# Optimization experiments

Measured on AMD Instinct MI355X. Metric: run time of the kernel, lower is better.

The kernel has to match this reference:

```python
import jax, jax.numpy as jnp
import numpy as np

N_HEADS = 12
N_GROUPS = 32
EPS = 1e-5


def setup_inputs() -> dict:
    key = jax.random.key(0)
    ks = jax.random.split(key, 6)
    B, C, H, W = 8, 768, 32, 32
    EC, S = 768, 256
    x = jax.random.normal(ks[0], (B, C, H, W), dtype=jnp.float32)
    encoder_out = jax.random.normal(ks[1], (B, EC, S), dtype=jnp.float32)
    gn_w = jnp.ones((C,), jnp.float32)
    gn_b = jnp.zeros((C,), jnp.float32)
    qkv_w = jax.random.normal(ks[2], (3 * C, C), dtype=jnp.float32) * 0.02
    qkv_b = jnp.zeros((3 * C,), jnp.float32)
    enc_w = jax.random.normal(ks[3], (2 * C, EC), dtype=jnp.float32) * 0.02
    enc_b = jnp.zeros((2 * C,), jnp.float32)
    proj_w = jax.random.normal(ks[4], (C, C), dtype=jnp.float32) * 0.02
    proj_b = jnp.zeros((C,), jnp.float32)
    return {"x": x, "encoder_out": encoder_out, "gn_w": gn_w, "gn_b": gn_b,
            "qkv_w": qkv_w, "qkv_b": qkv_b, "enc_w": enc_w, "enc_b": enc_b,
            "proj_w": proj_w, "proj_b": proj_b}


def _group_norm(x, w, b):
    # x: [B, C, T]
    B, C, T = x.shape
    xg = x.reshape(B, N_GROUPS, C // N_GROUPS, T)
    mean = jnp.mean(xg, axis=(2, 3), keepdims=True)
    var = jnp.var(xg, axis=(2, 3), keepdims=True)
    xn = ((xg - mean) * jax.lax.rsqrt(var + EPS)).reshape(B, C, T)
    return xn * w[None, :, None] + b[None, :, None]


def reference(x, encoder_out, gn_w, gn_b, qkv_w, qkv_b, enc_w, enc_b, proj_w, proj_b):
    B, C, Hs, Ws = x.shape
    T = Hs * Ws
    ch = C // N_HEADS
    xf = x.reshape(B, C, T)
    xn = _group_norm(xf, gn_w, gn_b)
    # 1x1 conv == channel matmul
    qkv = jnp.einsum('oc,bct->bot', qkv_w, xn) + qkv_b[None, :, None]  # [B, 3C, T]
    # torch layout: per-head contiguous blocks of [q, k, v]
    qkv = qkv.reshape(B * N_HEADS, 3 * ch, T)
    q, k, v = qkv[:, :ch], qkv[:, ch:2 * ch], qkv[:, 2 * ch:]
    ekv = jnp.einsum('oc,bcs->bos', enc_w, encoder_out) + enc_b[None, :, None]  # [B, 2C, S]
    ekv = ekv.reshape(B * N_HEADS, 2 * ch, -1)
    ek, ev = ekv[:, :ch], ekv[:, ch:]
    k = jnp.concatenate([ek, k], axis=-1)  # [BH, ch, S+T]
    v = jnp.concatenate([ev, v], axis=-1)
    scale = 1.0 / np.sqrt(np.sqrt(ch))
    w = jnp.einsum('bct,bcs->bts', q * scale, k * scale)  # [BH, T, S+T]
    w = jax.nn.softmax(w.astype(jnp.float32), axis=-1).astype(q.dtype)
    a = jnp.einsum('bts,bcs->bct', w, v).reshape(B, C, T)
    h = jnp.einsum('oc,bct->bot', proj_w, a) + proj_b[None, :, None]
    return (xf + h).reshape(B, C, Hs, Ws)
```

## Files before the change

kernel.cpp:

```cpp
#include <hip/hip_runtime.h>

typedef __attribute__((ext_vector_type(8))) short bf16x8;
typedef __attribute__((ext_vector_type(4))) float f32x4;
typedef __attribute__((ext_vector_type(16))) float f32x16;
typedef __attribute__((ext_vector_type(4))) float float4v;
typedef __attribute__((ext_vector_type(4))) unsigned short ushort4v;
typedef __attribute__((ext_vector_type(8))) unsigned short ushort8v;

#define DEVINL __device__ __forceinline__


DEVINL unsigned short f2bf(float f) {
  union { float f; unsigned u; } v; v.f = f;
  unsigned r = (v.u + 0x7fffu + ((v.u >> 16) & 1u)) >> 16;
  return (unsigned short)r;
}
DEVINL float bf2f(unsigned short h) {
  union { unsigned u; float f; } v; v.u = ((unsigned)h) << 16;
  return v.f;
}
DEVINL float exp2a(float x) {
  float r; asm("v_exp_f32 %0, %1" : "=v"(r) : "v"(x)); return r;
}
DEVINL unsigned cvtpk(float lo, float hi) {
  unsigned r;
  asm("v_cvt_pk_bf16_f32 %0, %1, %2" : "=v"(r) : "v"(lo), "v"(hi));
  return r;
}
DEVINL void gload16(const void* g, void* l) {
  __builtin_amdgcn_global_load_lds(
      (const __attribute__((address_space(1))) unsigned*)g,
      (__attribute__((address_space(3))) unsigned*)l, 16, 0, 0);
}
DEVINL void plswap(unsigned& a, unsigned& b) {
  asm("v_permlane32_swap_b32 %0, %1" : "+v"(a), "+v"(b));
}
DEVINL bf16x8 mkfrag(unsigned a, unsigned b, unsigned c, unsigned d) {
  union { unsigned u[4]; bf16x8 v; } x;
  x.u[0] = a; x.u[1] = b; x.u[2] = c; x.u[3] = d;
  return x.v;
}
#define WAITV0 asm volatile("s_waitcnt vmcnt(0)" ::: "memory")
#define RBAR  __builtin_amdgcn_s_barrier()

__global__ __launch_bounds__(256) void k_cvt3(const float* __restrict__ s0,
                                              const float* __restrict__ s1,
                                              const float* __restrict__ s2,
                                              unsigned short* __restrict__ d) {
  int i = blockIdx.x * 256 + threadIdx.x;
  const float* s; int off;
  if (i < 442368)      { s = s0; off = i; }
  else if (i < 737280) { s = s1; off = i - 442368; }
  else                 { s = s2; off = i - 737280; }
  float4v v = *(const float4v*)(s + (size_t)off * 4);
  ushort4v o;
  o[0] = f2bf(v[0]); o[1] = f2bf(v[1]); o[2] = f2bf(v[2]); o[3] = f2bf(v[3]);
  *(ushort4v*)(d + (size_t)i * 4) = o;
}

__global__ __launch_bounds__(256) void k_gn(const float* __restrict__ x,
                                            const float* __restrict__ gw,
                                            const float* __restrict__ gb,
                                            unsigned short* __restrict__ xnt) {
  int g = blockIdx.x, b = blockIdx.y, tid = threadIdx.x;
  const float* xb = x + ((size_t)b * 768 + g * 24) * 1024;
  float s = 0.f, ss = 0.f;
  for (int i = tid; i < 6144; i += 256) {
    float4v v = *(const float4v*)(xb + (size_t)i * 4);
    s += v[0] + v[1] + v[2] + v[3];
    ss += v[0] * v[0] + v[1] * v[1] + v[2] * v[2] + v[3] * v[3];
  }
  #pragma unroll
  for (int o = 32; o > 0; o >>= 1) { s += __shfl_down(s, o); ss += __shfl_down(ss, o); }
  __shared__ float rs[4], rss[4], stat[2];
  int w = tid >> 6;
  if ((tid & 63) == 0) { rs[w] = s; rss[w] = ss; }
  __syncthreads();
  if (tid == 0) {
    float S = rs[0] + rs[1] + rs[2] + rs[3], SS = rss[0] + rss[1] + rss[2] + rss[3];
    float mean = S / 24576.f;
    float var = SS / 24576.f - mean * mean;
    stat[0] = mean; stat[1] = rsqrtf(fmaxf(var, 0.f) + 1e-5f);
  }
  __syncthreads();
  float mean = stat[0], rstd = stat[1];
  float wv[24], bv[24];
  #pragma unroll
  for (int c = 0; c < 24; ++c) { wv[c] = gw[g * 24 + c]; bv[c] = gb[g * 24 + c]; }
  for (int it = 0; it < 4; ++it) {
    int t = it * 256 + tid;
    ushort8v ov[3];
    #pragma unroll
    for (int c = 0; c < 24; ++c) {
      float v = xb[(size_t)c * 1024 + t];
      ov[c >> 3][c & 7] = f2bf((v - mean) * rstd * wv[c] + bv[c]);
    }
    ushort8v* dst = (ushort8v*)(xnt + ((size_t)(b * 1024 + t)) * 768 + g * 24);
    dst[0] = ov[0]; dst[1] = ov[1]; dst[2] = ov[2];
  }
}

__global__ __launch_bounds__(256) void k_enc_tr(const float* __restrict__ enc,
                                                unsigned short* __restrict__ et) {
  int ct = blockIdx.x * 64, st = blockIdx.y * 64, b = blockIdx.z, tid = threadIdx.x;
  __shared__ unsigned short L[64 * 72];
  #pragma unroll
  for (int it = 0; it < 4; ++it) {
    int idx = it * 256 + tid; int r = idx >> 4, ch = idx & 15;
    float4v v = *(const float4v*)(enc + ((size_t)(b * 768 + ct + r)) * 256 + st + ch * 4);
    ushort4v o;
    o[0] = f2bf(v[0]); o[1] = f2bf(v[1]); o[2] = f2bf(v[2]); o[3] = f2bf(v[3]);
    *(ushort4v*)&L[r * 72 + ch * 4] = o;
  }
  __syncthreads();
  #pragma unroll
  for (int it = 0; it < 2; ++it) {
    int idx = it * 256 + tid; int s = idx >> 3, ch = idx & 7;
    ushort8v o;
    #pragma unroll
    for (int j = 0; j < 8; ++j) o[j] = L[(ch * 8 + j) * 72 + s];
    *(ushort8v*)(et + ((size_t)(b * 256 + st + s)) * 768 + ct + ch * 8) = o;
  }
}

__global__ __launch_bounds__(256) void k_vcat(const unsigned short* __restrict__ qkvt,
                                              const unsigned short* __restrict__ ekvt,
                                              unsigned short* __restrict__ vcat) {
  int s0 = blockIdx.x * 64, bh = blockIdx.y, b = bh / 12, h = bh % 12, tid = threadIdx.x;
  __shared__ unsigned short L[64 * 72];
  #pragma unroll
  for (int it = 0; it < 2; ++it) {
    int idx = it * 256 + tid; int s = idx >> 3, ch = idx & 7;
    int sg = s0 + s;
    const unsigned short* src = (sg < 256)
        ? ekvt + ((size_t)(b * 256 + sg)) * 1536 + h * 128 + 64 + ch * 8
        : qkvt + ((size_t)(b * 1024 + sg - 256)) * 2304 + h * 192 + 128 + ch * 8;
    *(ushort8v*)&L[s * 72 + ch * 8] = *(const ushort8v*)src;
  }
  __syncthreads();
  #pragma unroll
  for (int it = 0; it < 2; ++it) {
    int idx = it * 256 + tid; int c = idx >> 3, ch = idx & 7;
    ushort8v o;
    #pragma unroll
    for (int j = 0; j < 8; ++j) o[j] = L[(ch * 8 + j) * 72 + c];
    *(ushort8v*)(vcat + ((size_t)bh * 64 + c) * 1280 + s0 + ch * 8) = o;
  }
}

template <int EPI, int BM>
__global__ __launch_bounds__(256, 3) void k_gemm(const unsigned short* __restrict__ A,
                                                 const unsigned short* __restrict__ B,
                                                 const float* __restrict__ bias,
                                                 const float* __restrict__ resid,
                                                 void* __restrict__ outp,
                                                 int N, int K,
                                                 long sA, long sB, long sO, long sR) {
  constexpr int R32 = BM / 64;
  int bz = blockIdx.z;
  int m0 = blockIdx.x * BM, n0 = blockIdx.y * 128;
  const unsigned short* Ab = A + (size_t)bz * sA + (size_t)m0 * K;
  const unsigned short* Bb = B + (size_t)bz * sB + (size_t)n0 * K;
  __shared__ unsigned short As[3][BM * 32], Bs[3][128 * 32];
  int tid = threadIdx.x, lane = tid & 63, w = tid >> 6;
  int l31 = lane & 31, hi2 = lane >> 5;
  int wm = (w >> 1) * (BM / 2), wn = (w & 1) * 64;
  int sr = tid >> 2, sc = tid & 3;
  int schunk = (sc ^ ((sr >> 1) & 3)) * 8;
  const unsigned short* gA = Ab + (size_t)sr * K + schunk;
  const unsigned short* gB = Bb + (size_t)sr * K + schunk;

  f32x16 acc[R32][2];
  #pragma unroll
  for (int i = 0; i < R32; ++i)
    #pragma unroll
    for (int j = 0; j < 2; ++j)
      #pragma unroll
      for (int r = 0; r < 16; ++r) acc[i][j][r] = 0.f;

  auto stageAB = [&](int buf, int k0) {
    unsigned short* ad = &As[buf][0] + w * 512;
    unsigned short* bd = &Bs[buf][0] + w * 512;
    gload16(gA + k0, ad);
    if constexpr (BM == 128) gload16(gA + (size_t)64 * K + k0, ad + 2048);
    gload16(gB + k0, bd);
    gload16(gB + (size_t)64 * K + k0, bd + 2048);
  };
  auto WAITP = [&] {
    if constexpr (BM == 128) asm volatile("s_waitcnt vmcnt(4)" ::: "memory");
    else                     asm volatile("s_waitcnt vmcnt(3)" ::: "memory");
  };
  auto comp = [&](int buf) {
    const char* abase = (const char*)&As[buf][0];
    const char* bbase = (const char*)&Bs[buf][0];
    #pragma unroll
    for (int kk = 0; kk < 2; ++kk) {
      bf16x8 afr[R32], bfr[2];
      #pragma unroll
      for (int ri = 0; ri < R32; ++ri) {
        int row = wm + ri * 32 + l31;
        int sl = (kk * 2 + hi2) ^ ((row >> 1) & 3);
        afr[ri] = *(const bf16x8*)(abase + row * 64 + sl * 16);
      }
      #pragma unroll
      for (int ci = 0; ci < 2; ++ci) {
        int row = wn + ci * 32 + l31;
        int sl = (kk * 2 + hi2) ^ ((row >> 1) & 3);
        bfr[ci] = *(const bf16x8*)(bbase + row * 64 + sl * 16);
      }
      #pragma unroll
      for (int ri = 0; ri < R32; ++ri)
        #pragma unroll
        for (int ci = 0; ci < 2; ++ci)
          acc[ri][ci] = __builtin_amdgcn_mfma_f32_32x32x16_bf16(afr[ri], bfr[ci],
                                                                acc[ri][ci], 0, 0, 0);
    }
  };

  int nk = K >> 5;
  stageAB(0, 0);
  stageAB(1, 32);
  WAITP();
  RBAR;
  int cur = 0;
  for (int kt = 0; kt < nk - 2; ++kt) {
    int pre = cur - 1; if (pre < 0) pre += 3;
    stageAB(pre, (kt + 2) * 32);
    comp(cur);
    WAITP();
    RBAR;
    ++cur; if (cur == 3) cur = 0;
  }
  comp(cur);
  WAITV0;
  RBAR;
  ++cur; if (cur == 3) cur = 0;
  comp(cur);

  #pragma unroll
  for (int ri = 0; ri < R32; ++ri) {
    #pragma unroll
    for (int ci = 0; ci < 2; ++ci) {
      #pragma unroll
      for (int rg = 0; rg < 16; ++rg) {
        int row = m0 + wm + ri * 32 + (rg & 3) + 8 * (rg >> 2) + 4 * hi2;
        int col = n0 + wn + ci * 32 + l31;
        float v = acc[ri][ci][rg];
        if (EPI == 0) {
          v += bias[col];
          ((unsigned short*)outp)[(size_t)bz * sO + (size_t)row * N + col] = f2bf(v);
        } else {
          v += bias[row] + resid[(size_t)bz * sR + (size_t)row * N + col];
          ((float*)outp)[(size_t)bz * sO + (size_t)row * N + col] = v;
        }
      }
    }
  }
}

__global__ __launch_bounds__(256, 3) void k_attn(const unsigned short* __restrict__ qkvt,
                                                 const unsigned short* __restrict__ ekvt,
                                                 const unsigned short* __restrict__ vcat,
                                                 unsigned short* __restrict__ at) {
  int bid = blockIdx.x;
  int swb = (bid & 7) * 96 + (bid >> 3);
  int t0 = (swb & 7) * 128, bh = swb >> 3, b = bh / 12, h = bh % 12;
  int tid = threadIdx.x, w = tid >> 6, lane = tid & 63;
  int ql = lane & 31, hi = lane >> 5;
  __shared__ unsigned short Ks[2][4096], Vs[2][4096];

  const float QSC = 0.125f * 1.44269504089f;
  bf16x8 aq[4];
  const unsigned short* qrow = qkvt + ((size_t)(b * 1024 + t0 + w * 32 + ql)) * 2304 + h * 192;
  #pragma unroll
  for (int jc = 0; jc < 4; ++jc) {
    ushort8v qv = *(const ushort8v*)(qrow + jc * 16 + hi * 8);
    bf16x8 o;
    #pragma unroll
    for (int e = 0; e < 8; ++e) o[e] = (short)f2bf(bf2f(qv[e]) * QSC);
    aq[jc] = o;
  }

  int rloc = w * 16 + (lane >> 3);
  int chunk = (lane & 7) ^ (lane >> 3);
  const unsigned short* ke_st = ekvt + ((size_t)(b * 256 + rloc)) * 1536 + h * 128 + chunk * 8;
  const unsigned short* kq_st = qkvt + ((long)b * 1024 - 256 + rloc) * 2304 + h * 192 + 64 + chunk * 8;
  const unsigned short* v_st  = vcat + ((size_t)(bh * 64 + rloc)) * 1280 + chunk * 8;
  unsigned short* kd = &Ks[0][0] + w * 1024;
  unsigned short* vd = &Vs[0][0] + w * 1024;

  auto stage = [&](int nb, int tn) {
    const unsigned short* ks;
    size_t rstep;
    if (tn < 4) { ks = ke_st + (size_t)tn * 64 * 1536; rstep = 8 * 1536; }
    else        { ks = kq_st + (size_t)tn * 64 * 2304; rstep = 8 * 2304; }
    unsigned short* kdd = kd + nb * 4096;
    unsigned short* vdd = vd + nb * 4096;
    const unsigned short* vs = v_st + tn * 64;
    gload16(ks, kdd);
    gload16(ks + rstep, kdd + 512);
    gload16(vs, vdd);
    gload16(vs + 8 * 1280, vdd + 512);
  };

  stage(0, 0);
  WAITV0;
  __syncthreads();

  f32x16 acc0, acc1;
  #pragma unroll
  for (int r = 0; r < 16; ++r) { acc0[r] = 0.f; acc1[r] = 0.f; }
  float l = 0.f;
  int xp = (ql & 7) << 4;

  for (int t = 0; t < 20; ++t) {
    int cur = t & 1;
    if (t < 19) stage(cur ^ 1, t + 1);

    f32x16 sf0, sf1;
    #pragma unroll
    for (int r = 0; r < 16; ++r) { sf0[r] = 0.f; sf1[r] = 0.f; }
    const char* kbase = (const char*)&Ks[cur][0] + ql * 128;
    __builtin_amdgcn_s_setprio(1);
    #pragma unroll
    for (int jc = 0; jc < 4; ++jc) {
      int off = (jc * 32 + hi * 16) ^ xp;
      bf16x8 k0f = *(const bf16x8*)(kbase + off);
      bf16x8 k1f = *(const bf16x8*)(kbase + 4096 + off);
      sf0 = __builtin_amdgcn_mfma_f32_32x32x16_bf16(k0f, aq[jc], sf0, 0, 0, 0);
      sf1 = __builtin_amdgcn_mfma_f32_32x32x16_bf16(k1f, aq[jc], sf1, 0, 0, 0);
    }
    __builtin_amdgcn_s_setprio(0);

    float pe[32];
    #pragma unroll
    for (int i = 0; i < 16; ++i) pe[i] = exp2a(sf0[i]);
    #pragma unroll
    for (int i = 0; i < 16; ++i) pe[16 + i] = exp2a(sf1[i]);

    const char* vbase = (const char*)&Vs[cur][0] + ql * 128;
    #pragma unroll
    for (int sb = 0; sb < 2; ++sb) {
      unsigned pk[8];
      #pragma unroll
      for (int i = 0; i < 8; ++i)
        pk[i] = cvtpk(pe[sb * 16 + 2 * i], pe[sb * 16 + 2 * i + 1]);
      plswap(pk[0], pk[2]);
      plswap(pk[1], pk[3]);
      plswap(pk[4], pk[6]);
      plswap(pk[5], pk[7]);
      bf16x8 fj0 = mkfrag(pk[0], pk[1], pk[2], pk[3]);
      bf16x8 fj1 = mkfrag(pk[4], pk[5], pk[6], pk[7]);
      __builtin_amdgcn_s_setprio(1);
      #pragma unroll
      for (int jj = 0; jj < 2; ++jj) {
        int off = (sb * 64 + jj * 32 + hi * 16) ^ xp;
        bf16x8 v0f = *(const bf16x8*)(vbase + off);
        bf16x8 v1f = *(const bf16x8*)(vbase + 4096 + off);
        bf16x8 pf = jj ? fj1 : fj0;
        acc0 = __builtin_amdgcn_mfma_f32_32x32x16_bf16(v0f, pf, acc0, 0, 0, 0);
        acc1 = __builtin_amdgcn_mfma_f32_32x32x16_bf16(v1f, pf, acc1, 0, 0, 0);
      }
      __builtin_amdgcn_s_setprio(0);
    }

    float s0 = 0.f, s1 = 0.f, s2 = 0.f, s3 = 0.f;
    #pragma unroll
    for (int i = 0; i < 8; ++i) {
      s0 += pe[i]; s1 += pe[8 + i]; s2 += pe[16 + i]; s3 += pe[24 + i];
    }
    l += (s0 + s1) + (s2 + s3);

    if (t < 19) WAITV0;
    __syncthreads();
  }

  l += __shfl_xor(l, 32);
  float rl = 1.f / l;
  unsigned short* orow = at + ((size_t)(b * 1024 + t0 + w * 32 + ql)) * 768 + h * 64;
  #pragma unroll
  for (int cb = 0; cb < 2; ++cb) {
    #pragma unroll
    for (int g = 0; g < 4; ++g) {
      int c = cb * 32 + g * 8 + hi * 4;
      ushort4v o;
      #pragma unroll
      for (int i = 0; i < 4; ++i) {
        float v = (cb ? acc1[g * 4 + i] : acc0[g * 4 + i]) * rl;
        o[i] = f2bf(v);
      }
      *(ushort4v*)(orow + c) = o;
    }
  }
}

extern "C" void kernel_launch(void* const* d_in, const int* in_sizes, int n_in,
                              void* d_out, int out_size, void* d_ws, size_t ws_size,
                              hipStream_t stream) {
  const float* x      = (const float*)d_in[0];
  const float* enc    = (const float*)d_in[1];
  const float* gn_w   = (const float*)d_in[2];
  const float* gn_b   = (const float*)d_in[3];
  const float* qkv_w  = (const float*)d_in[4];
  const float* qkv_b  = (const float*)d_in[5];
  const float* enc_w  = (const float*)d_in[6];
  const float* enc_b  = (const float*)d_in[7];
  const float* proj_w = (const float*)d_in[8];
  const float* proj_b = (const float*)d_in[9];
  float* out = (float*)d_out;

  char* ws = (char*)d_ws;
  unsigned short* w_qkv = (unsigned short*)(ws + 0);
  unsigned short* w_enc = (unsigned short*)(ws + 3538944);
  unsigned short* w_prj = (unsigned short*)(ws + 5898240);
  unsigned short* xn_t  = (unsigned short*)(ws + 7077888);
  unsigned short* enc_t = (unsigned short*)(ws + 19660800);
  unsigned short* qkv_t = (unsigned short*)(ws + 22806528);
  unsigned short* ekv_t = (unsigned short*)(ws + 60555264);
  unsigned short* vcat  = (unsigned short*)(ws + 66846720);
  unsigned short* a_t   = xn_t;

  k_cvt3<<<3456, 256, 0, stream>>>(qkv_w, enc_w, proj_w, w_qkv);
  k_gn<<<dim3(32, 8), 256, 0, stream>>>(x, gn_w, gn_b, xn_t);
  k_enc_tr<<<dim3(12, 4, 8), 256, 0, stream>>>(enc, enc_t);
  k_gemm<0, 128><<<dim3(64, 18, 1), 256, 0, stream>>>(xn_t, w_qkv, qkv_b, nullptr, qkv_t,
                                                      2304, 768, 0L, 0L, 0L, 0L);
  k_gemm<0, 64><<<dim3(32, 12, 1), 256, 0, stream>>>(enc_t, w_enc, enc_b, nullptr, ekv_t,
                                                     1536, 768, 0L, 0L, 0L, 0L);
  k_vcat<<<dim3(20, 96), 256, 0, stream>>>(qkv_t, ekv_t, vcat);
  k_attn<<<dim3(768), 256, 0, stream>>>(qkv_t, ekv_t, vcat, a_t);
  k_gemm<1, 64><<<dim3(12, 8, 8), 256, 0, stream>>>(w_prj, a_t, proj_b, x, out,
                                                    1024, 768, 0L, 786432L, 786432L, 786432L);
}
```

Baseline: 168.1 us.

## Merge prep kernels and QKV/enc GEMMs; process two query tiles per attention block

Folds the weight conversion, group norm and encoder transpose into one launch, and merges the QKV and encoder-KV GEMMs into one grid, with the encoder GEMM switched to 128-row tiles. This removes launch gaps and tail underutilisation between small kernels. The attention kernel now handles 256 query rows per block in two 128-row halves that share each staged K/V tile, halving the block count and K/V LDS traffic per query. The exp and row-sum are fused into the P-pack loop. The cost is more register pressure in attention and fewer attention blocks (384) to fill the GPU.

```diff
diff --git a/kernel.cpp b/kernel.cpp
--- a/kernel.cpp
+++ b/kernel.cpp
@@ -41,69 +41,76 @@
   return x.v;
 }
 #define WAITV0 asm volatile("s_waitcnt vmcnt(0)" ::: "memory")
+#define WAITV3 asm volatile("s_waitcnt vmcnt(3)" ::: "memory")
+#define WAITV4 asm volatile("s_waitcnt vmcnt(4)" ::: "memory")
 #define RBAR  __builtin_amdgcn_s_barrier()
 
-__global__ __launch_bounds__(256) void k_cvt3(const float* __restrict__ s0,
+__global__ __launch_bounds__(256) void k_prep(const float* __restrict__ s0,
                                               const float* __restrict__ s1,
                                               const float* __restrict__ s2,
-                                              unsigned short* __restrict__ d) {
-  int i = blockIdx.x * 256 + threadIdx.x;
-  const float* s; int off;
-  if (i < 442368)      { s = s0; off = i; }
-  else if (i < 737280) { s = s1; off = i - 442368; }
-  else                 { s = s2; off = i - 737280; }
-  float4v v = *(const float4v*)(s + (size_t)off * 4);
-  ushort4v o;
-  o[0] = f2bf(v[0]); o[1] = f2bf(v[1]); o[2] = f2bf(v[2]); o[3] = f2bf(v[3]);
-  *(ushort4v*)(d + (size_t)i * 4) = o;
-}
-
-__global__ __launch_bounds__(256) void k_gn(const float* __restrict__ x,
-                                            const float* __restrict__ gw,
-                                            const float* __restrict__ gb,
-                                            unsigned short* __restrict__ xnt) {
-  int g = blockIdx.x, b = blockIdx.y, tid = threadIdx.x;
-  const float* xb = x + ((size_t)b * 768 + g * 24) * 1024;
-  float s = 0.f, ss = 0.f;
-  for (int i = tid; i < 6144; i += 256) {
-    float4v v = *(const float4v*)(xb + (size_t)i * 4);
-    s += v[0] + v[1] + v[2] + v[3];
-    ss += v[0] * v[0] + v[1] * v[1] + v[2] * v[2] + v[3] * v[3];
-  }
-  #pragma unroll
-  for (int o = 32; o > 0; o >>= 1) { s += __shfl_down(s, o); ss += __shfl_down(ss, o); }
+                                              unsigned short* __restrict__ wd,
+                                              const float* __restrict__ x,
+                                              const float* __restrict__ gw,
+                                              const float* __restrict__ gb,
+                                              unsigned short* __restrict__ xnt,
+                                              const float* __restrict__ enc,
+                                              unsigned short* __restrict__ et) {
+  __shared__ unsigned short L[64 * 72];
   __shared__ float rs[4], rss[4], stat[2];
-  int w = tid >> 6;
-  if ((tid & 63) == 0) { rs[w] = s; rss[w] = ss; }
-  __syncthreads();
-  if (tid == 0) {
-    float S = rs[0] + rs[1] + rs[2] + rs[3], SS = rss[0] + rss[1] + rss[2] + rss[3];
-    float mean = S / 24576.f;
-    float var = SS / 24576.f - mean * mean;
-    stat[0] = mean; stat[1] = rsqrtf(fmaxf(var, 0.f) + 1e-5f);
-  }
-  __syncthreads();
-  float mean = stat[0], rstd = stat[1];
-  float wv[24], bv[24];
-  #pragma unroll
-  for (int c = 0; c < 24; ++c) { wv[c] = gw[g * 24 + c]; bv[c] = gb[g * 24 + c]; }
-  for (int it = 0; it < 4; ++it) {
-    int t = it * 256 + tid;
-    ushort8v ov[3];
-    #pragma unroll
-    for (int c = 0; c < 24; ++c) {
-      float v = xb[(size_t)c * 1024 + t];
-      ov[c >> 3][c & 7] = f2bf((v - mean) * rstd * wv[c] + bv[c]);
-    }
-    ushort8v* dst = (ushort8v*)(xnt + ((size_t)(b * 1024 + t)) * 768 + g * 24);
-    dst[0] = ov[0]; dst[1] = ov[1]; dst[2] = ov[2];
-  }
-}
-
-__global__ __launch_bounds__(256) void k_enc_tr(const float* __restrict__ enc,
-                                                unsigned short* __restrict__ et) {
-  int ct = blockIdx.x * 64, st = blockIdx.y * 64, b = blockIdx.z, tid = threadIdx.x;
-  __shared__ unsigned short L[64 * 72];
+  int blk = blockIdx.x, tid = threadIdx.x;
+
+  if (blk < 3456) {
+    int i = blk * 256 + tid;
+    const float* s; int off;
+    if (i < 442368)      { s = s0; off = i; }
+    else if (i < 737280) { s = s1; off = i - 442368; }
+    else                 { s = s2; off = i - 737280; }
+    float4v v = *(const float4v*)(s + (size_t)off * 4);
+    ushort4v o;
+    o[0] = f2bf(v[0]); o[1] = f2bf(v[1]); o[2] = f2bf(v[2]); o[3] = f2bf(v[3]);
+    *(ushort4v*)(wd + (size_t)i * 4) = o;
+    return;
+  }
+  if (blk < 3712) {
+    int e = blk - 3456, g = e & 31, b = e >> 5;
+    const float* xb = x + ((size_t)b * 768 + g * 24) * 1024;
+    float s = 0.f, ss = 0.f;
+    for (int i = tid; i < 6144; i += 256) {
+      float4v v = *(const float4v*)(xb + (size_t)i * 4);
+      s += v[0] + v[1] + v[2] + v[3];
+      ss += v[0] * v[0] + v[1] * v[1] + v[2] * v[2] + v[3] * v[3];
+    }
+    #pragma unroll
+    for (int o = 32; o > 0; o >>= 1) { s += __shfl_down(s, o); ss += __shfl_down(ss, o); }
+    int wv_ = tid >> 6;
+    if ((tid & 63) == 0) { rs[wv_] = s; rss[wv_] = ss; }
+    __syncthreads();
+    if (tid == 0) {
+      float S = rs[0] + rs[1] + rs[2] + rs[3], SS = rss[0] + rss[1] + rss[2] + rss[3];
+      float mean = S / 24576.f;
+      float var = SS / 24576.f - mean * mean;
+      stat[0] = mean; stat[1] = rsqrtf(fmaxf(var, 0.f) + 1e-5f);
+    }
+    __syncthreads();
+    float mean = stat[0], rstd = stat[1];
+    float wv[24], bv[24];
+    #pragma unroll
+    for (int c = 0; c < 24; ++c) { wv[c] = gw[g * 24 + c]; bv[c] = gb[g * 24 + c]; }
+    for (int it = 0; it < 4; ++it) {
+      int t = it * 256 + tid;
+      ushort8v ov[3];
+      #pragma unroll
+      for (int c = 0; c < 24; ++c) {
+        float v = xb[(size_t)c * 1024 + t];
+        ov[c >> 3][c & 7] = f2bf((v - mean) * rstd * wv[c] + bv[c]);
+      }
+      ushort8v* dst = (ushort8v*)(xnt + ((size_t)(b * 1024 + t)) * 768 + g * 24);
+      dst[0] = ov[0]; dst[1] = ov[1]; dst[2] = ov[2];
+    }
+    return;
+  }
+  int e = blk - 3712;
+  int ct = (e % 12) * 64, st = ((e / 12) & 3) * 64, b = e / 48;
   #pragma unroll
   for (int it = 0; it < 4; ++it) {
     int idx = it * 256 + tid; int r = idx >> 4, ch = idx & 15;
@@ -148,31 +155,39 @@
   }
 }
 
-template <int EPI, int BM>
-__global__ __launch_bounds__(256, 3) void k_gemm(const unsigned short* __restrict__ A,
-                                                 const unsigned short* __restrict__ B,
-                                                 const float* __restrict__ bias,
-                                                 const float* __restrict__ resid,
-                                                 void* __restrict__ outp,
-                                                 int N, int K,
-                                                 long sA, long sB, long sO, long sR) {
-  constexpr int R32 = BM / 64;
-  int bz = blockIdx.z;
-  int m0 = blockIdx.x * BM, n0 = blockIdx.y * 128;
-  const unsigned short* Ab = A + (size_t)bz * sA + (size_t)m0 * K;
-  const unsigned short* Bb = B + (size_t)bz * sB + (size_t)n0 * K;
-  __shared__ unsigned short As[3][BM * 32], Bs[3][128 * 32];
+__global__ __launch_bounds__(256, 3) void k_g12(const unsigned short* __restrict__ A1,
+                                                const unsigned short* __restrict__ B1,
+                                                const float* __restrict__ bias1,
+                                                unsigned short* __restrict__ out1,
+                                                const unsigned short* __restrict__ A2,
+                                                const unsigned short* __restrict__ B2,
+                                                const float* __restrict__ bias2,
+                                                unsigned short* __restrict__ out2) {
+  const int K = 768;
+  int gid = blockIdx.x;
+  const unsigned short *A, *Bp; const float* bias; unsigned short* outp; int N, m0, n0;
+  if (gid < 1152) {
+    A = A1; Bp = B1; bias = bias1; outp = out1; N = 2304;
+    m0 = (gid & 63) * 128; n0 = (gid >> 6) * 128;
+  } else {
+    int g = gid - 1152;
+    A = A2; Bp = B2; bias = bias2; outp = out2; N = 1536;
+    m0 = (g & 15) * 128; n0 = (g >> 4) * 128;
+  }
+  const unsigned short* Ab = A + (size_t)m0 * K;
+  const unsigned short* Bb = Bp + (size_t)n0 * K;
+  __shared__ unsigned short As[3][4096], Bs[3][4096];
   int tid = threadIdx.x, lane = tid & 63, w = tid >> 6;
   int l31 = lane & 31, hi2 = lane >> 5;
-  int wm = (w >> 1) * (BM / 2), wn = (w & 1) * 64;
+  int wm = (w >> 1) * 64, wn = (w & 1) * 64;
   int sr = tid >> 2, sc = tid & 3;
   int schunk = (sc ^ ((sr >> 1) & 3)) * 8;
   const unsigned short* gA = Ab + (size_t)sr * K + schunk;
   const unsigned short* gB = Bb + (size_t)sr * K + schunk;
 
-  f32x16 acc[R32][2];
-  #pragma unroll
-  for (int i = 0; i < R32; ++i)
+  f32x16 acc[2][2];
+  #pragma unroll
+  for (int i = 0; i < 2; ++i)
     #pragma unroll
     for (int j = 0; j < 2; ++j)
       #pragma unroll
@@ -182,22 +197,18 @@
     unsigned short* ad = &As[buf][0] + w * 512;
     unsigned short* bd = &Bs[buf][0] + w * 512;
     gload16(gA + k0, ad);
-    if constexpr (BM == 128) gload16(gA + (size_t)64 * K + k0, ad + 2048);
+    gload16(gA + (size_t)64 * K + k0, ad + 2048);
     gload16(gB + k0, bd);
     gload16(gB + (size_t)64 * K + k0, bd + 2048);
-  };
-  auto WAITP = [&] {
-    if constexpr (BM == 128) asm volatile("s_waitcnt vmcnt(4)" ::: "memory");
-    else                     asm volatile("s_waitcnt vmcnt(3)" ::: "memory");
   };
   auto comp = [&](int buf) {
     const char* abase = (const char*)&As[buf][0];
     const char* bbase = (const char*)&Bs[buf][0];
     #pragma unroll
     for (int kk = 0; kk < 2; ++kk) {
-      bf16x8 afr[R32], bfr[2];
-      #pragma unroll
-      for (int ri = 0; ri < R32; ++ri) {
+      bf16x8 afr[2], bfr[2];
+      #pragma unroll
+      for (int ri = 0; ri < 2; ++ri) {
         int row = wm + ri * 32 + l31;
         int sl = (kk * 2 + hi2) ^ ((row >> 1) & 3);
         afr[ri] = *(const bf16x8*)(abase + row * 64 + sl * 16);
@@ -209,7 +220,7 @@
         bfr[ci] = *(const bf16x8*)(bbase + row * 64 + sl * 16);
       }
       #pragma unroll
-      for (int ri = 0; ri < R32; ++ri)
+      for (int ri = 0; ri < 2; ++ri)
         #pragma unroll
         for (int ci = 0; ci < 2; ++ci)
           acc[ri][ci] = __builtin_amdgcn_mfma_f32_32x32x16_bf16(afr[ri], bfr[ci],
@@ -217,17 +228,106 @@
     }
   };
 
+  stageAB(0, 0);
+  stageAB(1, 32);
+  WAITV4;
+  RBAR;
+  int cur = 0;
+  for (int kt = 0; kt < 22; ++kt) {
+    int pre = cur - 1; if (pre < 0) pre += 3;
+    stageAB(pre, (kt + 2) * 32);
+    comp(cur);
+    WAITV4;
+    RBAR;
+    ++cur; if (cur == 3) cur = 0;
+  }
+  comp(cur);
+  WAITV0;
+  RBAR;
+  ++cur; if (cur == 3) cur = 0;
+  comp(cur);
+
+  #pragma unroll
+  for (int ri = 0; ri < 2; ++ri) {
+    #pragma unroll
+    for (int ci = 0; ci < 2; ++ci) {
+      #pragma unroll
+      for (int rg = 0; rg < 16; ++rg) {
+        int row = m0 + wm + ri * 32 + (rg & 3) + 8 * (rg >> 2) + 4 * hi2;
+        int col = n0 + wn + ci * 32 + l31;
+        outp[(size_t)row * N + col] = f2bf(acc[ri][ci][rg] + bias[col]);
+      }
+    }
+  }
+}
+
+__global__ __launch_bounds__(256, 3) void k_gemm3(const unsigned short* __restrict__ A,
+                                                  const unsigned short* __restrict__ B,
+                                                  const float* __restrict__ bias,
+                                                  const float* __restrict__ resid,
+                                                  float* __restrict__ outp,
+                                                  int N, int K,
+                                                  long sB, long sO, long sR) {
+  int bz = blockIdx.z;
+  int m0 = blockIdx.x * 64, n0 = blockIdx.y * 128;
+  const unsigned short* Ab = A + (size_t)m0 * K;
+  const unsigned short* Bb = B + (size_t)bz * sB + (size_t)n0 * K;
+  __shared__ unsigned short As[3][2048], Bs[3][4096];
+  int tid = threadIdx.x, lane = tid & 63, w = tid >> 6;
+  int l31 = lane & 31, hi2 = lane >> 5;
+  int wm = (w >> 1) * 32, wn = (w & 1) * 64;
+  int sr = tid >> 2, sc = tid & 3;
+  int schunk = (sc ^ ((sr >> 1) & 3)) * 8;
+  const unsigned short* gA = Ab + (size_t)sr * K + schunk;
+  const unsigned short* gB = Bb + (size_t)sr * K + schunk;
+
+  f32x16 acc[2];
+  #pragma unroll
+  for (int j = 0; j < 2; ++j)
+    #pragma unroll
+    for (int r = 0; r < 16; ++r) acc[j][r] = 0.f;
+
+  auto stageAB = [&](int buf, int k0) {
+    unsigned short* ad = &As[buf][0] + w * 512;
+    unsigned short* bd = &Bs[buf][0] + w * 512;
+    gload16(gA + k0, ad);
+    gload16(gB + k0, bd);
+    gload16(gB + (size_t)64 * K + k0, bd + 2048);
+  };
+  auto comp = [&](int buf) {
+    const char* abase = (const char*)&As[buf][0];
+    const char* bbase = (const char*)&Bs[buf][0];
+    #pragma unroll
+    for (int kk = 0; kk < 2; ++kk) {
+      bf16x8 afr, bfr[2];
+      {
+        int row = wm + l31;
+        int sl = (kk * 2 + hi2) ^ ((row >> 1) & 3);
+        afr = *(const bf16x8*)(abase + row * 64 + sl * 16);
+      }
+      #pragma unroll
+      for (int ci = 0; ci < 2; ++ci) {
+        int row = wn + ci * 32 + l31;
+        int sl = (kk * 2 + hi2) ^ ((row >> 1) & 3);
+        bfr[ci] = *(const bf16x8*)(bbase + row * 64 + sl * 16);
+      }
+      #pragma unroll
+      for (int ci = 0; ci < 2; ++ci)
+        acc[ci] = __builtin_amdgcn_mfma_f32_32x32x16_bf16(afr, bfr[ci], acc[ci], 0, 0, 0);
+    }
+  };
+
   int nk = K >> 5;
   stageAB(0, 0);
   stageAB(1, 32);
-  WAITP();
+  WAITV3;
   RBAR;
   int cur = 0;
   for (int kt = 0; kt < nk - 2; ++kt) {
     int pre = cur - 1; if (pre < 0) pre += 3;
     stageAB(pre, (kt + 2) * 32);
     comp(cur);
-    WAITP();
+    WAITV3;
     RBAR;
     ++cur; if (cur == 3) cur = 0;
   }
@@ -238,22 +338,13 @@
   comp(cur);
 
   #pragma unroll
-  for (int ri = 0; ri < R32; ++ri) {
-    #pragma unroll
-    for (int ci = 0; ci < 2; ++ci) {
-      #pragma unroll
-      for (int rg = 0; rg < 16; ++rg) {
-        int row = m0 + wm + ri * 32 + (rg & 3) + 8 * (rg >> 2) + 4 * hi2;
-        int col = n0 + wn + ci * 32 + l31;
-        float v = acc[ri][ci][rg];
-        if (EPI == 0) {
-          v += bias[col];
-          ((unsigned short*)outp)[(size_t)bz * sO + (size_t)row * N + col] = f2bf(v);
-        } else {
-          v += bias[row] + resid[(size_t)bz * sR + (size_t)row * N + col];
-          ((float*)outp)[(size_t)bz * sO + (size_t)row * N + col] = v;
-        }
-      }
+  for (int ci = 0; ci < 2; ++ci) {
+    #pragma unroll
+    for (int rg = 0; rg < 16; ++rg) {
+      int row = m0 + wm + (rg & 3) + 8 * (rg >> 2) + 4 * hi2;
+      int col = n0 + wn + ci * 32 + l31;
+      float v = acc[ci][rg] + bias[row] + resid[(size_t)bz * sR + (size_t)row * N + col];
+      outp[(size_t)bz * sO + (size_t)row * N + col] = v;
     }
   }
 }
@@ -263,22 +354,27 @@
                                                  const unsigned short* __restrict__ vcat,
                                                  unsigned short* __restrict__ at) {
   int bid = blockIdx.x;
-  int swb = (bid & 7) * 96 + (bid >> 3);
-  int t0 = (swb & 7) * 128, bh = swb >> 3, b = bh / 12, h = bh % 12;
+  int swb = (bid & 7) * 48 + (bid >> 3);
+  int bh = swb >> 2, tq = (swb & 3) * 256;
+  int b = bh / 12, h = bh % 12;
   int tid = threadIdx.x, w = tid >> 6, lane = tid & 63;
   int ql = lane & 31, hi = lane >> 5;
   __shared__ unsigned short Ks[2][4096], Vs[2][4096];
 
   const float QSC = 0.125f * 1.44269504089f;
-  bf16x8 aq[4];
-  const unsigned short* qrow = qkvt + ((size_t)(b * 1024 + t0 + w * 32 + ql)) * 2304 + h * 192;
+  bf16x8 aqA[4], aqB[4];
+  const unsigned short* qrowA = qkvt + ((size_t)(b * 1024 + tq + w * 32 + ql)) * 2304 + h * 192;
   #pragma unroll
   for (int jc = 0; jc < 4; ++jc) {
-    ushort8v qv = *(const ushort8v*)(qrow + jc * 16 + hi * 8);
-    bf16x8 o;
-    #pragma unroll
-    for (int e = 0; e < 8; ++e) o[e] = (short)f2bf(bf2f(qv[e]) * QSC);
-    aq[jc] = o;
+    ushort8v qv = *(const ushort8v*)(qrowA + jc * 16 + hi * 8);
+    ushort8v qw = *(const ushort8v*)(qrowA + (size_t)128 * 2304 + jc * 16 + hi * 8);
+    bf16x8 oa, ob;
+    #pragma unroll
+    for (int e = 0; e < 8; ++e) {
+      oa[e] = (short)f2bf(bf2f(qv[e]) * QSC);
+      ob[e] = (short)f2bf(bf2f(qw[e]) * QSC);
+    }
+    aqA[jc] = oa; aqB[jc] = ob;
   }
 
   int rloc = w * 16 + (lane >> 3);
@@ -307,16 +403,13 @@
   WAITV0;
   __syncthreads();
 
-  f32x16 acc0, acc1;
-  #pragma unroll
-  for (int r = 0; r < 16; ++r) { acc0[r] = 0.f; acc1[r] = 0.f; }
-  float l = 0.f;
+  f32x16 accA0, accA1, accB0, accB1;
+  #pragma unroll
+  for (int r = 0; r < 16; ++r) { accA0[r] = 0.f; accA1[r] = 0.f; accB0[r] = 0.f; accB1[r] = 0.f; }
+  float lA = 0.f, lB = 0.f;
   int xp = (ql & 7) << 4;
 
-  for (int t = 0; t < 20; ++t) {
-    int cur = t & 1;
-    if (t < 19) stage(cur ^ 1, t + 1);
-
+  auto tilebody = [&](const bf16x8* aqv, f32x16& a0, f32x16& a1, float& lv, int cur) {
     f32x16 sf0, sf1;
     #pragma unroll
     for (int r = 0; r < 16; ++r) { sf0[r] = 0.f; sf1[r] = 0.f; }
@@ -327,24 +420,21 @@
       int off = (jc * 32 + hi * 16) ^ xp;
       bf16x8 k0f = *(const bf16x8*)(kbase + off);
       bf16x8 k1f = *(const bf16x8*)(kbase + 4096 + off);
-      sf0 = __builtin_amdgcn_mfma_f32_32x32x16_bf16(k0f, aq[jc], sf0, 0, 0, 0);
-      sf1 = __builtin_amdgcn_mfma_f32_32x32x16_bf16(k1f, aq[jc], sf1, 0, 0, 0);
+      sf0 = __builtin_amdgcn_mfma_f32_32x32x16_bf16(k0f, aqv[jc], sf0, 0, 0, 0);
+      sf1 = __builtin_amdgcn_mfma_f32_32x32x16_bf16(k1f, aqv[jc], sf1, 0, 0, 0);
     }
     __builtin_amdgcn_s_setprio(0);
-
-    float pe[32];
-    #pragma unroll
-    for (int i = 0; i < 16; ++i) pe[i] = exp2a(sf0[i]);
-    #pragma unroll
-    for (int i = 0; i < 16; ++i) pe[16 + i] = exp2a(sf1[i]);
-
     const char* vbase = (const char*)&Vs[cur][0] + ql * 128;
     #pragma unroll
     for (int sb = 0; sb < 2; ++sb) {
       unsigned pk[8];
       #pragma unroll
-      for (int i = 0; i < 8; ++i)
-        pk[i] = cvtpk(pe[sb * 16 + 2 * i], pe[sb * 16 + 2 * i + 1]);
+      for (int i = 0; i < 8; ++i) {
+        float ea = exp2a(sb ? sf1[2 * i] : sf0[2 * i]);
+        float eb = exp2a(sb ? sf1[2 * i + 1] : sf0[2 * i + 1]);
+        lv += ea + eb;
+        pk[i] = cvtpk(ea, eb);
+      }
       plswap(pk[0], pk[2]);
       plswap(pk[1], pk[3]);
       plswap(pk[4], pk[6]);
@@ -358,38 +448,40 @@
         bf16x8 v0f = *(const bf16x8*)(vbase + off);
         bf16x8 v1f = *(const bf16x8*)(vbase + 4096 + off);
         bf16x8 pf = jj ? fj1 : fj0;
-        acc0 = __builtin_amdgcn_mfma_f32_32x32x16_bf16(v0f, pf, acc0, 0, 0, 0);
-        acc1 = __builtin_amdgcn_mfma_f32_32x32x16_bf16(v1f, pf, acc1, 0, 0, 0);
+        a0 = __builtin_amdgcn_mfma_f32_32x32x16_bf16(v0f, pf, a0, 0, 0, 0);
+        a1 = __builtin_amdgcn_mfma_f32_32x32x16_bf16(v1f, pf, a1, 0, 0, 0);
       }
       __builtin_amdgcn_s_setprio(0);
     }
-
-    float s0 = 0.f, s1 = 0.f, s2 = 0.f, s3 = 0.f;
-    #pragma unroll
-    for (int i = 0; i < 8; ++i) {
-      s0 += pe[i]; s1 += pe[8 + i]; s2 += pe[16 + i]; s3 += pe[24 + i];
-    }
-    l += (s0 + s1) + (s2 + s3);
-
+  };
+
+  for (int t = 0; t < 20; ++t) {
+    int cur = t & 1;
+    if (t < 19) stage(cur ^ 1, t + 1);
+    tilebody(aqA, accA0, accA1, lA, cur);
+    tilebody(aqB, accB0, accB1, lB, cur);
     if (t < 19) WAITV0;
     __syncthreads();
   }
 
-  l += __shfl_xor(l, 32);
-  float rl = 1.f / l;
-  unsigned short* orow = at + ((size_t)(b * 1024 + t0 + w * 32 + ql)) * 768 + h * 64;
+  lA += __shfl_xor(lA, 32);
+  lB += __shfl_xor(lB, 32);
+  float rlA = 1.f / lA, rlB = 1.f / lB;
+  unsigned short* orowA = at + ((size_t)(b * 1024 + tq + w * 32 + ql)) * 768 + h * 64;
+  unsigned short* orowB = orowA + (size_t)128 * 768;
   #pragma unroll
   for (int cb = 0; cb < 2; ++cb) {
     #pragma unroll
     for (int g = 0; g < 4; ++g) {
       int c = cb * 32 + g * 8 + hi * 4;
-      ushort4v o;
+      ushort4v oa, ob;
       #pragma unroll
       for (int i = 0; i < 4; ++i) {
-        float v = (cb ? acc1[g * 4 + i] : acc0[g * 4 + i]) * rl;
-        o[i] = f2bf(v);
-      }
-      *(ushort4v*)(orow + c) = o;
+        oa[i] = f2bf((cb ? accA1[g * 4 + i] : accA0[g * 4 + i]) * rlA);
+        ob[i] = f2bf((cb ? accB1[g * 4 + i] : accB0[g * 4 + i]) * rlB);
+      }
+      *(ushort4v*)(orowA + c) = oa;
+      *(ushort4v*)(orowB + c) = ob;
     }
   }
 }
@@ -420,15 +512,12 @@
   unsigned short* vcat  = (unsigned short*)(ws + 66846720);
   unsigned short* a_t   = xn_t;
 
-  k_cvt3<<<3456, 256, 0, stream>>>(qkv_w, enc_w, proj_w, w_qkv);
-  k_gn<<<dim3(32, 8), 256, 0, stream>>>(x, gn_w, gn_b, xn_t);
-  k_enc_tr<<<dim3(12, 4, 8), 256, 0, stream>>>(enc, enc_t);
-  k_gemm<0, 128><<<dim3(64, 18, 1), 256, 0, stream>>>(xn_t, w_qkv, qkv_b, nullptr, qkv_t,
-                                                      2304, 768, 0L, 0L, 0L, 0L);
-  k_gemm<0, 64><<<dim3(32, 12, 1), 256, 0, stream>>>(enc_t, w_enc, enc_b, nullptr, ekv_t,
-                                                     1536, 768, 0L, 0L, 0L, 0L);
+  k_prep<<<4096, 256, 0, stream>>>(qkv_w, enc_w, proj_w, w_qkv,
+                                   x, gn_w, gn_b, xn_t, enc, enc_t);
+  k_g12<<<1344, 256, 0, stream>>>(xn_t, w_qkv, qkv_b, qkv_t,
+                                  enc_t, w_enc, enc_b, ekv_t);
   k_vcat<<<dim3(20, 96), 256, 0, stream>>>(qkv_t, ekv_t, vcat);
-  k_attn<<<dim3(768), 256, 0, stream>>>(qkv_t, ekv_t, vcat, a_t);
-  k_gemm<1, 64><<<dim3(12, 8, 8), 256, 0, stream>>>(w_prj, a_t, proj_b, x, out,
-                                                    1024, 768, 0L, 786432L, 786432L, 786432L);
-}
+  k_attn<<<dim3(384), 256, 0, stream>>>(qkv_t, ekv_t, vcat, a_t);
+  k_gemm3<<<dim3(12, 8, 8), 256, 0, stream>>>(w_prj, a_t, proj_b, x, out,
+                                              1024, 768, 786432L, 786432L, 786432L);
+}
```

Result: slower. 227.5 us (+35.4%).
